# Optimization experiments

Hardware: AMD Instinct MI355X
Metric: run time of the kernel (lower is better)

Reference implementation:

```python
import jax, jax.numpy as jnp
import numpy as np

NUM_NODES = 2048
NUM_REL = 8
HIDDEN = 256


def setup_inputs() -> dict:
    key = jax.random.key(0)
    k1, k2, k3 = jax.random.split(key, 3)
    X = jax.random.normal(k1, (NUM_NODES, HIDDEN, NUM_REL), dtype=jnp.float32)
    A = jax.random.uniform(k2, (NUM_NODES, NUM_NODES, NUM_REL), dtype=jnp.float32)
    # nn.init.normal_(std=0.01)
    weight = 0.01 * jax.random.normal(k3, (HIDDEN, HIDDEN, NUM_REL), dtype=jnp.float32)
    return {"X": X, "A": A, "weight": weight}


def _tensor_product(A, B):
    # Faithful to the original: FFT along last (relation) dim, take REAL part of
    # both transformed operands, per-slice matmul, then real part of ifft.
    Af = jnp.real(jnp.fft.fft(A, axis=-1))  # (n1, n2, k)
    Bf = jnp.real(jnp.fft.fft(B, axis=-1))  # (n2, n4, k)
    C = jnp.einsum('nmk,mhk->nhk', Af, Bf)  # batched real matmul over slices k
    return jnp.real(jnp.fft.ifft(C, axis=-1)).astype(A.dtype)


def reference(X, A, weight):
    res = _tensor_product(A, X)          # (num_nodes, hidden, num_rel)
    res = _tensor_product(res, weight)   # (num_nodes, hidden, num_rel)
    return res
```

## Files before the change

kernel.cpp:

```cpp
#include <hip/hip_runtime.h>


typedef __bf16 bf16_t;
typedef __bf16 bf16x2 __attribute__((ext_vector_type(2)));
typedef __bf16 bf16x8 __attribute__((ext_vector_type(8)));
typedef float f32x4 __attribute__((ext_vector_type(4)));

#define R2C 0.70710678118654752f

__device__ __forceinline__ void fwd5(const float x[8], float F[5]) {
  float s04 = x[0] + x[4], d04 = x[0] - x[4];
  float s26 = x[2] + x[6];
  float s15 = x[1] + x[5], s37 = x[3] + x[7];
  float t = (x[1] + x[7]) - (x[3] + x[5]);
  float e = s04 + s26, o = s15 + s37;
  F[0] = e + o;
  F[1] = d04 + R2C * t;
  F[2] = s04 - s26;
  F[3] = d04 - R2C * t;
  F[4] = e - o;
}

__global__ __launch_bounds__(256) void k_pre(const float* __restrict__ X,
                                             const float* __restrict__ A,
                                             const float* __restrict__ W,
                                             bf16_t* __restrict__ Xft,
                                             bf16_t* __restrict__ Af,
                                             bf16_t* __restrict__ Wft) {
  int b = blockIdx.x;
  if (b < 8192) {
    size_t t = (size_t)b * 256 + threadIdx.x;
    size_t idx = t * 2;
    const float4* p = (const float4*)(A + idx * 8);
    float4 q0 = p[0], q1 = p[1], q2 = p[2], q3 = p[3];
    float x0[8] = {q0.x, q0.y, q0.z, q0.w, q1.x, q1.y, q1.z, q1.w};
    float x1[8] = {q2.x, q2.y, q2.z, q2.w, q3.x, q3.y, q3.z, q3.w};
    float F0[5], F1[5];
    fwd5(x0, F0);
    fwd5(x1, F1);
#pragma unroll
    for (int j = 0; j < 5; j++) {
      bf16x2 v = {(bf16_t)F0[j], (bf16_t)F1[j]};
      *(bf16x2*)(Af + (size_t)j * 4194304 + idx) = v;
    }
  } else if (b < 9216) {
    size_t t = (size_t)(b - 8192) * 256 + threadIdx.x;
    int h = (int)(t >> 10);
    int m = (int)(t & 1023) * 2;
    const float4* p0 = (const float4*)(X + ((size_t)m * 256 + h) * 8);
    const float4* p1 = (const float4*)(X + ((size_t)(m + 1) * 256 + h) * 8);
    float4 a0 = p0[0], b0 = p0[1], a1 = p1[0], b1 = p1[1];
    float x0[8] = {a0.x, a0.y, a0.z, a0.w, b0.x, b0.y, b0.z, b0.w};
    float x1[8] = {a1.x, a1.y, a1.z, a1.w, b1.x, b1.y, b1.z, b1.w};
    float F0[5], F1[5];
    fwd5(x0, F0);
    fwd5(x1, F1);
    size_t base = (size_t)h * 2048 + m;
#pragma unroll
    for (int j = 0; j < 5; j++) {
      bf16x2 v = {(bf16_t)F0[j], (bf16_t)F1[j]};
      *(bf16x2*)(Xft + (size_t)j * 524288 + base) = v;
    }
  } else {
    int h = b - 9216;
    int hp = threadIdx.x;
    const float4* p = (const float4*)(W + ((size_t)hp * 256 + h) * 8);
    float4 a = p[0], bb = p[1];
    float x[8] = {a.x, a.y, a.z, a.w, bb.x, bb.y, bb.z, bb.w};
    float F[5];
    fwd5(x, F);
    const float sc[5] = {0.125f, 0.25f, 0.25f, 0.25f, 0.125f};
    size_t base = (size_t)h * 256 + hp;
#pragma unroll
    for (int j = 0; j < 5; j++)
      Wft[(size_t)j * 65536 + base] = (bf16_t)(F[j] * sc[j]);
  }
}

__global__ __launch_bounds__(256) void gemm_k(const bf16_t* __restrict__ A,
                                              const bf16_t* __restrict__ B,
                                              float* __restrict__ C, int K,
                                              int KS, size_t ap, size_t bp,
                                              size_t cp) {
  __shared__ bf16_t As[128 * 64];
  __shared__ bf16_t Bs[128 * 64];
  const int z = blockIdx.z, j = z % 5, s = z / 5;
  const bf16_t* Aj = A + (size_t)j * ap;
  const bf16_t* Bj = B + (size_t)j * bp;
  float* Cj = C + (size_t)z * cp;
  const int n0 = blockIdx.x * 128, h0 = blockIdx.y * 128;
  const int tid = threadIdx.x;
  const int wv = tid >> 6, ln = tid & 63;
  const int quad = ln >> 4, l16 = ln & 15;
  const int wn = (wv & 1) * 64, wh = (wv >> 1) * 64;
  const int k0 = s * KS, k1 = k0 + KS;

  const bf16_t* pa[4];
  const bf16_t* pb[4];
  int dsts[4];
#pragma unroll
  for (int t = 0; t < 4; t++) {
    int slot = tid + t * 256;
    int row = slot >> 3, c16 = slot & 7;
    dsts[t] = row * 64 + ((c16 ^ (row & 7)) << 3);
    pa[t] = Aj + (size_t)(n0 + row) * K + k0 + c16 * 8;
    pb[t] = Bj + (size_t)(h0 + row) * K + k0 + c16 * 8;
  }
  uint4 va[4], vb[4];
#pragma unroll
  for (int t = 0; t < 4; t++) {
    va[t] = *(const uint4*)pa[t];
    vb[t] = *(const uint4*)pb[t];
  }

  f32x4 acc[4][4] = {};
  for (int kk = k0; kk < k1; kk += 64) {
    __syncthreads();
#pragma unroll
    for (int t = 0; t < 4; t++) {
      *(uint4*)(As + dsts[t]) = va[t];
      *(uint4*)(Bs + dsts[t]) = vb[t];
    }
    __syncthreads();
    if (kk + 64 < k1) {
#pragma unroll
      for (int t = 0; t < 4; t++) {
        pa[t] += 64;
        pb[t] += 64;
        va[t] = *(const uint4*)pa[t];
        vb[t] = *(const uint4*)pb[t];
      }
    }
#pragma unroll
    for (int kh = 0; kh < 2; kh++) {
      bf16x8 af[4], bfr[4];
      int c16 = kh * 4 + quad;
#pragma unroll
      for (int i = 0; i < 4; i++) {
        int ra = wn + i * 16 + l16;
        int rb = wh + i * 16 + l16;
        af[i] = *(const bf16x8*)(As + ra * 64 + ((c16 ^ (ra & 7)) << 3));
        bfr[i] = *(const bf16x8*)(Bs + rb * 64 + ((c16 ^ (rb & 7)) << 3));
      }
#pragma unroll
      for (int i = 0; i < 4; i++)
#pragma unroll
        for (int t = 0; t < 4; t++)
          acc[i][t] = __builtin_amdgcn_mfma_f32_16x16x32_bf16(af[i], bfr[t],
                                                              acc[i][t], 0, 0, 0);
    }
  }
#pragma unroll
  for (int i = 0; i < 4; i++) {
#pragma unroll
    for (int t = 0; t < 4; t++) {
      int hc = h0 + wh + t * 16 + l16;
#pragma unroll
      for (int rg = 0; rg < 4; rg++) {
        int nr = n0 + wn + i * 16 + quad * 4 + rg;
        Cj[(size_t)nr * 256 + hc] = acc[i][t][rg];
      }
    }
  }
}

__global__ __launch_bounds__(256) void k_red(const float* __restrict__ C1p,
                                             bf16_t* __restrict__ C1) {
  size_t idx = ((size_t)blockIdx.x * 256 + threadIdx.x) * 2;
  float2 a0 = *(const float2*)(C1p + idx);
  float2 a1 = *(const float2*)(C1p + 2621440 + idx);
  float2 a2 = *(const float2*)(C1p + 2 * 2621440 + idx);
  float2 a3 = *(const float2*)(C1p + 3 * 2621440 + idx);
  bf16x2 v = {(bf16_t)(a0.x + a1.x + a2.x + a3.x),
              (bf16_t)(a0.y + a1.y + a2.y + a3.y)};
  *(bf16x2*)(C1 + idx) = v;
}

__global__ __launch_bounds__(256) void k_combine(const float* __restrict__ C2,
                                                 float* __restrict__ out) {
  size_t idx = (size_t)blockIdx.x * 256 + threadIdx.x;
  float c0 = C2[idx];
  float c1 = C2[524288 + idx];
  float c2 = C2[2 * 524288 + idx];
  float c3 = C2[3 * 524288 + idx];
  float c4 = C2[4 * 524288 + idx];
  float o0 = c0 + c1 + c2 + c3 + c4;
  float o4 = c0 - c1 + c2 - c3 + c4;
  float o2 = c0 - c2 + c4;
  float rt = R2C * (c1 - c3);
  float o1 = c0 + rt - c4;
  float o3 = c0 - rt - c4;
  float4* op = (float4*)(out + idx * 8);
  op[0] = make_float4(o0, o1, o2, o3);
  op[1] = make_float4(o4, o3, o2, o1);
}

extern "C" void kernel_launch(void* const* d_in, const int* in_sizes, int n_in,
                              void* d_out, int out_size, void* d_ws, size_t ws_size,
                              hipStream_t stream) {
  const float* X = (const float*)d_in[0];
  const float* A = (const float*)d_in[1];
  const float* W = (const float*)d_in[2];
  float* out = (float*)d_out;
  char* ws = (char*)d_ws;

  bf16_t* Af  = (bf16_t*)(ws);
  bf16_t* Xft = (bf16_t*)(ws + 41943040);
  bf16_t* Wft = (bf16_t*)(ws + 47185920);
  float*  C1p = (float*) (ws + 47841280);
  bf16_t* C1  = (bf16_t*)(ws + 89784320);
  float*  C2  = (float*) (ws + 95027200);

  k_pre<<<dim3(9472), 256, 0, stream>>>(X, A, W, Xft, Af, Wft);
  gemm_k<<<dim3(16, 2, 20), 256, 0, stream>>>(Af, Xft, C1p, 2048, 512,
                                              (size_t)4194304, (size_t)524288,
                                              (size_t)524288);
  k_red<<<dim3(5120), 256, 0, stream>>>(C1p, C1);
  gemm_k<<<dim3(16, 2, 5), 256, 0, stream>>>(C1, Wft, C2, 256, 256,
                                             (size_t)524288, (size_t)65536,
                                             (size_t)524288);
  k_combine<<<dim3(2048), 256, 0, stream>>>(C2, out);
}
```

Before: 312.6 us.

## Pre-swizzle GEMM operands globally, use direct global-to-LDS loads, drop split-K

```diff
diff --git a/kernel.cpp b/kernel.cpp
--- a/kernel.cpp
+++ b/kernel.cpp
@@ -7,6 +7,16 @@
 typedef float f32x4 __attribute__((ext_vector_type(4)));
 
 #define R2C 0.70710678118654752f
+
+__device__ __forceinline__ size_t swz(int r, int c, int K) {
+  return (size_t)r * K + (c & ~63) + ((((c >> 3) & 7) ^ (r & 7)) << 3) + (c & 7);
+}
+
+__device__ __forceinline__ void async_cp16(const void* g, void* l) {
+  __builtin_amdgcn_global_load_lds((const __attribute__((address_space(1))) char*)g,
+                                   (__attribute__((address_space(3))) char*)l,
+                                   16, 0, 0);
+}
 
 __device__ __forceinline__ void fwd5(const float x[8], float F[5]) {
   float s04 = x[0] + x[4], d04 = x[0] - x[4];
@@ -31,6 +41,7 @@
   if (b < 8192) {
     size_t t = (size_t)b * 256 + threadIdx.x;
     size_t idx = t * 2;
+    int n = (int)(idx >> 11), m = (int)(idx & 2047);
     const float4* p = (const float4*)(A + idx * 8);
     float4 q0 = p[0], q1 = p[1], q2 = p[2], q3 = p[3];
     float x0[8] = {q0.x, q0.y, q0.z, q0.w, q1.x, q1.y, q1.z, q1.w};
@@ -38,28 +49,28 @@
     float F0[5], F1[5];
     fwd5(x0, F0);
     fwd5(x1, F1);
+    size_t pos = swz(n, m, 2048);
 #pragma unroll
     for (int j = 0; j < 5; j++) {
       bf16x2 v = {(bf16_t)F0[j], (bf16_t)F1[j]};
-      *(bf16x2*)(Af + (size_t)j * 4194304 + idx) = v;
+      *(bf16x2*)(Af + (size_t)j * 4194304 + pos) = v;
     }
   } else if (b < 9216) {
     size_t t = (size_t)(b - 8192) * 256 + threadIdx.x;
-    int h = (int)(t >> 10);
-    int m = (int)(t & 1023) * 2;
-    const float4* p0 = (const float4*)(X + ((size_t)m * 256 + h) * 8);
-    const float4* p1 = (const float4*)(X + ((size_t)(m + 1) * 256 + h) * 8);
-    float4 a0 = p0[0], b0 = p0[1], a1 = p1[0], b1 = p1[1];
-    float x0[8] = {a0.x, a0.y, a0.z, a0.w, b0.x, b0.y, b0.z, b0.w};
-    float x1[8] = {a1.x, a1.y, a1.z, a1.w, b1.x, b1.y, b1.z, b1.w};
-    float F0[5], F1[5];
-    fwd5(x0, F0);
-    fwd5(x1, F1);
-    size_t base = (size_t)h * 2048 + m;
-#pragma unroll
-    for (int j = 0; j < 5; j++) {
-      bf16x2 v = {(bf16_t)F0[j], (bf16_t)F1[j]};
-      *(bf16x2*)(Xft + (size_t)j * 524288 + base) = v;
+    size_t p0 = t * 2;
+#pragma unroll
+    for (int u = 0; u < 2; u++) {
+      size_t pp = p0 + u;
+      int m = (int)(pp >> 8), h = (int)(pp & 255);
+      const float4* p = (const float4*)(X + pp * 8);
+      float4 a = p[0], bb = p[1];
+      float x[8] = {a.x, a.y, a.z, a.w, bb.x, bb.y, bb.z, bb.w};
+      float F[5];
+      fwd5(x, F);
+      size_t pos = swz(h, m, 2048);
+#pragma unroll
+      for (int j = 0; j < 5; j++)
+        Xft[(size_t)j * 524288 + pos] = (bf16_t)F[j];
     }
   } else {
     int h = b - 9216;
@@ -70,67 +81,54 @@
     float F[5];
     fwd5(x, F);
     const float sc[5] = {0.125f, 0.25f, 0.25f, 0.25f, 0.125f};
-    size_t base = (size_t)h * 256 + hp;
+    size_t pos = swz(h, hp, 256);
 #pragma unroll
     for (int j = 0; j < 5; j++)
-      Wft[(size_t)j * 65536 + base] = (bf16_t)(F[j] * sc[j]);
-  }
-}
-
-__global__ __launch_bounds__(256) void gemm_k(const bf16_t* __restrict__ A,
-                                              const bf16_t* __restrict__ B,
-                                              float* __restrict__ C, int K,
-                                              int KS, size_t ap, size_t bp,
-                                              size_t cp) {
+      Wft[(size_t)j * 65536 + pos] = (bf16_t)(F[j] * sc[j]);
+  }
+}
+
+template <typename OutT, bool SWZ_OUT>
+__global__ __launch_bounds__(256) void gemm_lds(const bf16_t* __restrict__ A,
+                                                const bf16_t* __restrict__ B,
+                                                OutT* __restrict__ C, int K,
+                                                size_t ap, size_t bp, size_t cp) {
   __shared__ bf16_t As[128 * 64];
   __shared__ bf16_t Bs[128 * 64];
-  const int z = blockIdx.z, j = z % 5, s = z / 5;
+  const int j = blockIdx.z;
   const bf16_t* Aj = A + (size_t)j * ap;
   const bf16_t* Bj = B + (size_t)j * bp;
-  float* Cj = C + (size_t)z * cp;
+  OutT* Cj = C + (size_t)j * cp;
   const int n0 = blockIdx.x * 128, h0 = blockIdx.y * 128;
   const int tid = threadIdx.x;
   const int wv = tid >> 6, ln = tid & 63;
   const int quad = ln >> 4, l16 = ln & 15;
   const int wn = (wv & 1) * 64, wh = (wv >> 1) * 64;
-  const int k0 = s * KS, k1 = k0 + KS;
-
-  const bf16_t* pa[4];
-  const bf16_t* pb[4];
-  int dsts[4];
-#pragma unroll
-  for (int t = 0; t < 4; t++) {
-    int slot = tid + t * 256;
+
+  const bf16_t* ga[4];
+  const bf16_t* gb[4];
+  bf16_t* la[4];
+  bf16_t* lb[4];
+#pragma unroll
+  for (int s = 0; s < 4; s++) {
+    int slot = s * 256 + tid;
     int row = slot >> 3, c16 = slot & 7;
-    dsts[t] = row * 64 + ((c16 ^ (row & 7)) << 3);
-    pa[t] = Aj + (size_t)(n0 + row) * K + k0 + c16 * 8;
-    pb[t] = Bj + (size_t)(h0 + row) * K + k0 + c16 * 8;
-  }
-  uint4 va[4], vb[4];
-#pragma unroll
-  for (int t = 0; t < 4; t++) {
-    va[t] = *(const uint4*)pa[t];
-    vb[t] = *(const uint4*)pb[t];
+    ga[s] = Aj + (size_t)(n0 + row) * K + c16 * 8;
+    gb[s] = Bj + (size_t)(h0 + row) * K + c16 * 8;
+    int base = (s * 256 + wv * 64) * 8;
+    la[s] = As + base;
+    lb[s] = Bs + base;
   }
 
   f32x4 acc[4][4] = {};
-  for (int kk = k0; kk < k1; kk += 64) {
+  for (int kk = 0; kk < K; kk += 64) {
     __syncthreads();
 #pragma unroll
-    for (int t = 0; t < 4; t++) {
-      *(uint4*)(As + dsts[t]) = va[t];
-      *(uint4*)(Bs + dsts[t]) = vb[t];
+    for (int s = 0; s < 4; s++) {
+      async_cp16(ga[s] + kk, la[s]);
+      async_cp16(gb[s] + kk, lb[s]);
     }
     __syncthreads();
-    if (kk + 64 < k1) {
-#pragma unroll
-      for (int t = 0; t < 4; t++) {
-        pa[t] += 64;
-        pb[t] += 64;
-        va[t] = *(const uint4*)pa[t];
-        vb[t] = *(const uint4*)pb[t];
-      }
-    }
 #pragma unroll
     for (int kh = 0; kh < 2; kh++) {
       bf16x8 af[4], bfr[4];
@@ -158,22 +156,11 @@
 #pragma unroll
       for (int rg = 0; rg < 4; rg++) {
         int nr = n0 + wn + i * 16 + quad * 4 + rg;
-        Cj[(size_t)nr * 256 + hc] = acc[i][t][rg];
+        size_t off = SWZ_OUT ? swz(nr, hc, 256) : (size_t)nr * 256 + hc;
+        Cj[off] = (OutT)acc[i][t][rg];
       }
     }
   }
-}
-
-__global__ __launch_bounds__(256) void k_red(const float* __restrict__ C1p,
-                                             bf16_t* __restrict__ C1) {
-  size_t idx = ((size_t)blockIdx.x * 256 + threadIdx.x) * 2;
-  float2 a0 = *(const float2*)(C1p + idx);
-  float2 a1 = *(const float2*)(C1p + 2621440 + idx);
-  float2 a2 = *(const float2*)(C1p + 2 * 2621440 + idx);
-  float2 a3 = *(const float2*)(C1p + 3 * 2621440 + idx);
-  bf16x2 v = {(bf16_t)(a0.x + a1.x + a2.x + a3.x),
-              (bf16_t)(a0.y + a1.y + a2.y + a3.y)};
-  *(bf16x2*)(C1 + idx) = v;
 }
 
 __global__ __launch_bounds__(256) void k_combine(const float* __restrict__ C2,
@@ -207,17 +194,13 @@
   bf16_t* Af  = (bf16_t*)(ws);
   bf16_t* Xft = (bf16_t*)(ws + 41943040);
   bf16_t* Wft = (bf16_t*)(ws + 47185920);
-  float*  C1p = (float*) (ws + 47841280);
-  bf16_t* C1  = (bf16_t*)(ws + 89784320);
-  float*  C2  = (float*) (ws + 95027200);
+  bf16_t* C1  = (bf16_t*)(ws + 47841280);
+  float*  C2  = (float*) (ws + 53084160);
 
   k_pre<<<dim3(9472), 256, 0, stream>>>(X, A, W, Xft, Af, Wft);
-  gemm_k<<<dim3(16, 2, 20), 256, 0, stream>>>(Af, Xft, C1p, 2048, 512,
-                                              (size_t)4194304, (size_t)524288,
-                                              (size_t)524288);
-  k_red<<<dim3(5120), 256, 0, stream>>>(C1p, C1);
-  gemm_k<<<dim3(16, 2, 5), 256, 0, stream>>>(C1, Wft, C2, 256, 256,
-                                             (size_t)524288, (size_t)65536,
-                                             (size_t)524288);
+  gemm_lds<bf16_t, true><<<dim3(16, 2, 5), 256, 0, stream>>>(
+      Af, Xft, C1, 2048, (size_t)4194304, (size_t)524288, (size_t)524288);
+  gemm_lds<float, false><<<dim3(16, 2, 5), 256, 0, stream>>>(
+      C1, Wft, C2, 256, (size_t)524288, (size_t)65536, (size_t)524288);
   k_combine<<<dim3(2048), 256, 0, stream>>>(C2, out);
 }
```

Result: faster. 288.4 us (-7.7%).
